# Optimization experiments

Hardware: AMD Instinct MI355X
Metric: run time of the kernel (lower is better)

The kernel has to match this reference:

```python
import jax, jax.numpy as jnp
import numpy as np

N = 100000      # nodes
E = 1600000     # edges (before self-loops)
NFEAT = 256
NHID = 64       # heads=1, concat -> output dim = NHID
NEG_SLOPE = 0.2 # PyG GATConv default negative_slope


def setup_inputs() -> dict:
    key = jax.random.key(0)
    k1, k2, k3, k4, k5 = jax.random.split(key, 5)
    x = jax.random.normal(k1, (N, NFEAT), dtype=jnp.float32)
    edge_index = jax.random.randint(k2, (2, E), 0, N, dtype=jnp.int64)
    s = 1.0 / np.sqrt(NFEAT)
    W = jax.random.uniform(k3, (NFEAT, NHID), jnp.float32, -s, s)      # lin weight
    a_src = jax.random.normal(k4, (NHID,), jnp.float32) * 0.1          # att_src
    a_dst = jax.random.normal(k5, (NHID,), jnp.float32) * 0.1          # att_dst
    bias = jnp.zeros((NHID,), jnp.float32)
    return {"x": x, "edge_index": edge_index, "W": W,
            "a_src": a_src, "a_dst": a_dst, "bias": bias}


def reference(x, edge_index, W, a_src, a_dst, bias):
    n = x.shape[0]
    xp = x @ W                                   # [N, NHID] transformed features
    # add self-loops (PyG default add_self_loops=True)
    loop = jnp.arange(n, dtype=edge_index.dtype)
    src = jnp.concatenate([edge_index[0], loop])  # message source j
    dst = jnp.concatenate([edge_index[1], loop])  # message target i
    # per-edge attention logits: LeakyReLU(a_src.x'_j + a_dst.x'_i)
    e = jax.nn.leaky_relu((xp @ a_src)[src] + (xp @ a_dst)[dst], NEG_SLOPE)  # [E+N]
    # segment softmax over incoming edges of each destination node
    m = jax.ops.segment_max(e, dst, num_segments=n)       # [N] (every node has a self-loop)
    ex = jnp.exp(e - m[dst])
    denom = jax.ops.segment_sum(ex, dst, num_segments=n)  # [N]
    alpha = ex / denom[dst]                                # [E+N]
    # attention-weighted scatter aggregation
    out = jax.ops.segment_sum(alpha[:, None] * xp[src], dst, num_segments=n)  # [N, NHID]
    return out + bias
```

## Files before the change

kernel.cpp:

```cpp
#include <hip/hip_runtime.h>
#include <hip/hip_bf16.h>

#define NFEAT 256
#define NHID  64
#define BSH   8
#define BUCKN 256
#define CAP   5120
#define CHUNK 4096

typedef unsigned int u32;
typedef unsigned short u16;
typedef long long ll;

typedef __attribute__((ext_vector_type(8))) short bf16x8;
typedef __attribute__((ext_vector_type(4))) float f32x4;

__device__ __forceinline__ float bfu2f(u16 u) {
    return __uint_as_float((u32)u << 16);
}
__device__ __forceinline__ u16 f2bfu(float f) {
    u32 u = __float_as_uint(f);
    u32 r = (u + 0x7fffu + ((u >> 16) & 1u)) >> 16;
    return (u16)r;
}
__device__ __forceinline__ float load_f(const void* p, int i, int f32) {
    return f32 ? ((const float*)p)[i] : bfu2f(((const u16*)p)[i]);
}

__device__ __forceinline__ void load_edge(const void* ei, int i64f, int E, int eid,
                                          int& src, int& dst) {
    if (eid < E) {
        if (i64f) {
            src = (int)((const ll*)ei)[eid];
            dst = (int)((const ll*)ei)[(size_t)E + eid];
        } else {
            src = ((const int*)ei)[eid];
            dst = ((const int*)ei)[(size_t)E + eid];
        }
    } else {
        src = dst = eid - E;
    }
}

__global__ __launch_bounds__(256) void prep_kernel(
    const void* __restrict__ W_, const void* __restrict__ ei,
    int* __restrict__ flags, u16* __restrict__ wt)
{
    __shared__ int f32sh;
    const int tid = threadIdx.x;
    if (tid == 0) f32sh = 0;
    __syncthreads();
    {
        float v = bfu2f(((const u16*)W_)[tid]);
        if (!(fabsf(v) <= 0.07f)) f32sh = 1;
    }
    if (tid < 64) {
        int v = ((const int*)ei)[2 * tid + 1];
        unsigned long long m = __ballot(v != 0);
        if (tid == 0) flags[1] = (m == 0ull) ? 1 : 0;
    }
    __syncthreads();
    const int f32 = f32sh;
    if (tid == 0) flags[0] = f32;
    for (int j = tid; j < NFEAT * NHID; j += 256) {
        int h = j >> 8, k = j & 255;
        wt[j] = f2bfu(load_f(W_, k * NHID + h, f32));
    }
}

__global__ __launch_bounds__(256) void gemm_kernel(
    const void* __restrict__ x_, const u16* __restrict__ wt,
    const void* __restrict__ a_src, const void* __restrict__ a_dst,
    const int* __restrict__ flags, u16* __restrict__ xpb,
    float* __restrict__ s, float* __restrict__ t_, int n)
{
    const int tid = threadIdx.x;
    const int lane = tid & 63;
    const int wv = tid >> 6;
    const int q = lane >> 4;
    const int l15 = lane & 15;
    const int f32 = flags[0];
    const int t = blockIdx.x;
    const int arow = min(t * 64 + wv * 16 + l15, n - 1);

    f32x4 acc[4] = {{0,0,0,0},{0,0,0,0},{0,0,0,0},{0,0,0,0}};
    const u16* wbase = wt + l15 * NFEAT + q * 8;

    if (f32) {
        const float* xb = (const float*)x_ + (size_t)arow * NFEAT + q * 8;
        #pragma unroll
        for (int ks = 0; ks < 8; ++ks) {
            float4 v0 = *(const float4*)(xb + ks * 32);
            float4 v1 = *(const float4*)(xb + ks * 32 + 4);
            bf16x8 a;
            a[0] = (short)f2bfu(v0.x); a[1] = (short)f2bfu(v0.y);
            a[2] = (short)f2bfu(v0.z); a[3] = (short)f2bfu(v0.w);
            a[4] = (short)f2bfu(v1.x); a[5] = (short)f2bfu(v1.y);
            a[6] = (short)f2bfu(v1.z); a[7] = (short)f2bfu(v1.w);
            #pragma unroll
            for (int tl = 0; tl < 4; ++tl) {
                bf16x8 b = *(const bf16x8*)(wbase + tl * 16 * NFEAT + ks * 32);
                acc[tl] = __builtin_amdgcn_mfma_f32_16x16x32_bf16(a, b, acc[tl], 0, 0, 0);
            }
        }
    } else {
        const u16* xb = (const u16*)x_ + (size_t)arow * NFEAT + q * 8;
        #pragma unroll
        for (int ks = 0; ks < 8; ++ks) {
            bf16x8 a = *(const bf16x8*)(xb + ks * 32);
            #pragma unroll
            for (int tl = 0; tl < 4; ++tl) {
                bf16x8 b = *(const bf16x8*)(wbase + tl * 16 * NFEAT + ks * 32);
                acc[tl] = __builtin_amdgcn_mfma_f32_16x16x32_bf16(a, b, acc[tl], 0, 0, 0);
            }
        }
    }

    float asl[4], adl[4];
    #pragma unroll
    for (int tl = 0; tl < 4; ++tl) {
        asl[tl] = load_f(a_src, tl * 16 + l15, f32);
        adl[tl] = load_f(a_dst, tl * 16 + l15, f32);
    }
    #pragma unroll
    for (int reg = 0; reg < 4; ++reg) {
        int node = t * 64 + wv * 16 + q * 4 + reg;
        bool ok = node < n;
        float pvs = 0.f, pvt = 0.f;
        #pragma unroll
        for (int tl = 0; tl < 4; ++tl) {
            float v = acc[tl][reg];
            if (ok) xpb[(size_t)node * NHID + tl * 16 + l15] = f2bfu(v);
            pvs = fmaf(v, asl[tl], pvs);
            pvt = fmaf(v, adl[tl], pvt);
        }
        #pragma unroll
        for (int o = 1; o < 16; o <<= 1) {
            pvs += __shfl_xor(pvs, o);
            pvt += __shfl_xor(pvt, o);
        }
        if (ok && l15 == 0) { s[node] = pvs; t_[node] = pvt; }
    }
}

__global__ __launch_bounds__(512) void bucket_kernel(
    const void* __restrict__ ei, const int* __restrict__ flags,
    int* __restrict__ gcursor, u32* __restrict__ rec, int E, int total)
{
    __shared__ int hist[512];
    __shared__ int offs[512];
    __shared__ int curs[512];
    __shared__ int gbase[512];
    __shared__ u32 stage[CHUNK];
    const int tid = threadIdx.x;
    const int base = blockIdx.x * CHUNK;
    const int cn = min(CHUNK, total - base);
    const int i64f = flags[1];

    hist[tid] = 0;
    __syncthreads();
    int es[8], ed[8];
    #pragma unroll
    for (int j = 0; j < 8; ++j) {
        int e = base + tid + 512 * j;
        if (e < total) {
            load_edge(ei, i64f, E, e, es[j], ed[j]);
            atomicAdd(&hist[ed[j] >> BSH], 1);
        } else ed[j] = -1;
    }
    __syncthreads();
    int v = hist[tid];
    offs[tid] = v;
    __syncthreads();
    for (int o = 1; o < 512; o <<= 1) {
        int tv = (tid >= o) ? offs[tid - o] : 0;
        __syncthreads();
        offs[tid] += tv;
        __syncthreads();
    }
    int excl = offs[tid] - v;
    __syncthreads();
    offs[tid] = excl;
    curs[tid] = excl;
    __syncthreads();
    #pragma unroll
    for (int j = 0; j < 8; ++j) {
        if (ed[j] >= 0) {
            int b = ed[j] >> BSH;
            int p = atomicAdd(&curs[b], 1);
            stage[p] = ((u32)(ed[j] & 255) << 24) | (u32)es[j];
        }
    }
    __syncthreads();
    {
        int b = tid;
        int nxt = (b < 511) ? offs[b + 1] : cn;
        int cb = nxt - offs[b];
        gbase[b] = b * CAP + (cb ? atomicAdd(&gcursor[b], cb) : 0);
    }
    __syncthreads();
    for (int i = tid; i < cn; i += 512) {
        u32 r = stage[i];
        int lo = 0, hi = 511;
        while (lo < hi) {
            int mid = (lo + hi + 1) >> 1;
            if (offs[mid] <= i) lo = mid; else hi = mid - 1;
        }
        rec[(size_t)gbase[lo] + (i - offs[lo])] = r;
    }
}

#define HN 128
__global__ __launch_bounds__(512) void fused_kernel(
    const u32* __restrict__ rec, const int* __restrict__ gcursor,
    const float* __restrict__ s, const float* __restrict__ t_,
    const u16* __restrict__ xpb, const void* __restrict__ bias,
    const int* __restrict__ flags, float* __restrict__ out, int n)
{
    __shared__ int rowp[HN + 1];
    __shared__ int curs[HN];
    __shared__ int ssrc[CAP * 3 / 4];
    const int b = blockIdx.x >> 1;
    const int half = blockIdx.x & 1;
    const int tid = threadIdx.x;
    const int dst0 = (b << BSH) + half * HN;
    const int cnt = min(gcursor[b], CAP);
    const u32* r = rec + (size_t)b * CAP;
    const int SCAP = CAP * 3 / 4;

    for (int i = tid; i <= HN; i += 512) rowp[i] = 0;
    __syncthreads();
    for (int i = tid; i < cnt; i += 512) {
        u32 v = r[i];
        int dl = (int)(v >> 24);
        if ((dl >> 7) == half) atomicAdd(&rowp[(dl & (HN - 1)) + 1], 1);
    }
    __syncthreads();
    for (int o = 1; o <= HN; o <<= 1) {
        int tv = 0;
        if (tid <= HN && tid >= o) tv = rowp[tid - o];
        __syncthreads();
        if (tid <= HN && tid >= o) rowp[tid] += tv;
        __syncthreads();
    }
    if (tid < HN) curs[tid] = rowp[tid];
    __syncthreads();
    for (int i = tid; i < cnt; i += 512) {
        u32 v = r[i];
        int dl = (int)(v >> 24);
        if ((dl >> 7) == half) {
            int p = atomicAdd(&curs[dl & (HN - 1)], 1);
            if (p < SCAP) ssrc[p] = (int)(v & 0x00FFFFFFu);
        }
    }
    __syncthreads();

    const int lane = tid & 63;
    const int wv = tid >> 6;
    const float bl = load_f(bias, lane, flags[0]);
    for (int nl = wv; nl < HN; nl += 8) {
        int node = dst0 + nl;
        if (node >= n) break;
        int beg = rowp[nl], end = min(rowp[nl + 1], SCAP);
        float tn = t_[node];
        float lsum = 0.f;
        float O0 = 0.f, O1 = 0.f, O2 = 0.f, O3 = 0.f;
        for (int j0 = beg; j0 < end; j0 += 64) {
            int c2 = min(64, end - j0);
            int sidx = 0; float p = 0.f;
            if (lane < c2) {
                sidx = ssrc[j0 + lane];
                float e = s[sidx] + tn;
                e = (e >= 0.f) ? e : 0.2f * e;
                p = __expf(e);
            }
            lsum += p;
            int jj = 0;
            for (; jj + 8 <= c2; jj += 8) {
                int sj[8]; float pj[8], rv[8];
                #pragma unroll
                for (int u = 0; u < 8; ++u) {
                    sj[u] = __shfl(sidx, jj + u);
                    pj[u] = __shfl(p, jj + u);
                }
                #pragma unroll
                for (int u = 0; u < 8; ++u)
                    rv[u] = bfu2f(xpb[(size_t)sj[u] * NHID + lane]);
                O0 = fmaf(pj[0], rv[0], O0); O1 = fmaf(pj[1], rv[1], O1);
                O2 = fmaf(pj[2], rv[2], O2); O3 = fmaf(pj[3], rv[3], O3);
                O0 = fmaf(pj[4], rv[4], O0); O1 = fmaf(pj[5], rv[5], O1);
                O2 = fmaf(pj[6], rv[6], O2); O3 = fmaf(pj[7], rv[7], O3);
            }
            for (; jj < c2; ++jj) {
                int s0 = __shfl(sidx, jj);
                float p0 = __shfl(p, jj);
                O0 = fmaf(p0, bfu2f(xpb[(size_t)s0 * NHID + lane]), O0);
            }
        }
        #pragma unroll
        for (int o = 32; o; o >>= 1) lsum += __shfl_xor(lsum, o);
        out[(size_t)node * NHID + lane] = ((O0 + O1) + (O2 + O3)) / lsum + bl;
    }
}

extern "C" void kernel_launch(void* const* d_in, const int* in_sizes, int n_in,
                              void* d_out, int out_size, void* d_ws, size_t ws_size,
                              hipStream_t stream) {
    const void* x     = d_in[0];
    const void* ei    = d_in[1];
    const void* W     = d_in[2];
    const void* a_src = d_in[3];
    const void* a_dst = d_in[4];
    const void* bias  = d_in[5];
    float* out = (float*)d_out;

    const int n     = in_sizes[0] / NFEAT;
    const int E     = in_sizes[1] / 2;
    const int total = E + n;
    const int NB    = (n + BUCKN - 1) >> BSH;
    const int NT    = (n + 63) / 64;

    char* ws = (char*)d_ws;
    size_t off = 0;
    auto carve = [&](size_t bytes) -> char* {
        char* p = ws + off;
        off = (off + bytes + 255) & ~(size_t)255;
        return p;
    };
    int*   flags   = (int*)  carve(64 * sizeof(int));
    u16*   wt      = (u16*)  carve((size_t)NFEAT * NHID * 2);
    u16*   xpb     = (u16*)  carve((size_t)n * NHID * 2);
    float* s       = (float*)carve((size_t)n * 4);
    float* t       = (float*)carve((size_t)n * 4);
    int*   gcursor = (int*)  carve(512 * 4);
    u32*   rec     = (u32*)  carve((size_t)NB * CAP * 4);

    hipMemsetAsync(gcursor, 0, 512 * 4, stream);

    prep_kernel<<<1, 256, 0, stream>>>(W, ei, flags, wt);
    gemm_kernel<<<NT, 256, 0, stream>>>(x, wt, a_src, a_dst, flags, xpb, s, t, n);
    bucket_kernel<<<(total + CHUNK - 1) / CHUNK, 512, 0, stream>>>(ei, flags, gcursor, rec, E, total);
    fused_kernel<<<NB * 2, 512, 0, stream>>>(rec, gcursor, s, t, xpb, bias, flags, out, n);
}
```

Measured before the change: 301.5 us.

## Replace bucketed edge staging with full CSR build via global count, scan, scatter

Replaces the two-level bucket sort (fixed-capacity buckets of 256 destinations, re-sorted in shared memory by each aggregation block) with a standard CSR construction. A global atomic degree count, a three-kernel prefix scan and a global atomic scatter produce per-node edge lists. The aggregation kernel then uses one wavefront per node in a grid-stride loop, reading sources straight from global memory. This removes the capacity truncation and the in-block sorting, but adds four extra launches and scattered global atomics on 100k counters, and edge order within a node becomes nondeterministic.

New measurement: 452.9 us. 1.5x slower.

```diff
diff --git a/kernel.cpp b/kernel.cpp
--- a/kernel.cpp
+++ b/kernel.cpp
@@ -3,10 +3,6 @@
 
 #define NFEAT 256
 #define NHID  64
-#define BSH   8
-#define BUCKN 256
-#define CAP   5120
-#define CHUNK 4096
 
 typedef unsigned int u32;
 typedef unsigned short u16;
@@ -143,133 +139,110 @@
     }
 }
 
-__global__ __launch_bounds__(512) void bucket_kernel(
+__global__ __launch_bounds__(256) void count_kernel(
     const void* __restrict__ ei, const int* __restrict__ flags,
-    int* __restrict__ gcursor, u32* __restrict__ rec, int E, int total)
-{
-    __shared__ int hist[512];
-    __shared__ int offs[512];
-    __shared__ int curs[512];
-    __shared__ int gbase[512];
-    __shared__ u32 stage[CHUNK];
-    const int tid = threadIdx.x;
-    const int base = blockIdx.x * CHUNK;
-    const int cn = min(CHUNK, total - base);
+    int* __restrict__ cnt, int E)
+{
     const int i64f = flags[1];
-
-    hist[tid] = 0;
-    __syncthreads();
-    int es[8], ed[8];
-    #pragma unroll
-    for (int j = 0; j < 8; ++j) {
-        int e = base + tid + 512 * j;
-        if (e < total) {
-            load_edge(ei, i64f, E, e, es[j], ed[j]);
-            atomicAdd(&hist[ed[j] >> BSH], 1);
-        } else ed[j] = -1;
-    }
-    __syncthreads();
-    int v = hist[tid];
-    offs[tid] = v;
+    const int stride = gridDim.x * 256;
+    for (int e = blockIdx.x * 256 + threadIdx.x; e < E; e += stride) {
+        int dst = i64f ? (int)((const ll*)ei)[(size_t)E + e]
+                       : ((const int*)ei)[(size_t)E + e];
+        atomicAdd(&cnt[dst], 1);
+    }
+}
+
+__global__ __launch_bounds__(256) void scan1_kernel(
+    const int* __restrict__ cnt, int* __restrict__ bsum, int n)
+{
+    __shared__ int sh[256];
+    const int t = threadIdx.x;
+    const int v = blockIdx.x * 256 + t;
+    sh[t] = (v < n) ? cnt[v] + 1 : 0;
+    __syncthreads();
+    for (int o = 128; o; o >>= 1) {
+        if (t < o) sh[t] += sh[t + o];
+        __syncthreads();
+    }
+    if (t == 0) bsum[blockIdx.x] = sh[0];
+}
+
+__global__ __launch_bounds__(512) void scan2_kernel(
+    const int* __restrict__ bsum, int* __restrict__ coff, int nc)
+{
+    __shared__ int sh[512];
+    const int t = threadIdx.x;
+    int mine = (t < nc) ? bsum[t] : 0;
+    sh[t] = mine;
     __syncthreads();
     for (int o = 1; o < 512; o <<= 1) {
-        int tv = (tid >= o) ? offs[tid - o] : 0;
-        __syncthreads();
-        offs[tid] += tv;
-        __syncthreads();
-    }
-    int excl = offs[tid] - v;
-    __syncthreads();
-    offs[tid] = excl;
-    curs[tid] = excl;
-    __syncthreads();
-    #pragma unroll
-    for (int j = 0; j < 8; ++j) {
-        if (ed[j] >= 0) {
-            int b = ed[j] >> BSH;
-            int p = atomicAdd(&curs[b], 1);
-            stage[p] = ((u32)(ed[j] & 255) << 24) | (u32)es[j];
-        }
-    }
-    __syncthreads();
-    {
-        int b = tid;
-        int nxt = (b < 511) ? offs[b + 1] : cn;
-        int cb = nxt - offs[b];
-        gbase[b] = b * CAP + (cb ? atomicAdd(&gcursor[b], cb) : 0);
-    }
-    __syncthreads();
-    for (int i = tid; i < cn; i += 512) {
-        u32 r = stage[i];
-        int lo = 0, hi = 511;
-        while (lo < hi) {
-            int mid = (lo + hi + 1) >> 1;
-            if (offs[mid] <= i) lo = mid; else hi = mid - 1;
-        }
-        rec[(size_t)gbase[lo] + (i - offs[lo])] = r;
-    }
-}
-
-#define HN 128
-__global__ __launch_bounds__(512) void fused_kernel(
-    const u32* __restrict__ rec, const int* __restrict__ gcursor,
+        int v = (t >= o) ? sh[t - o] : 0;
+        __syncthreads();
+        sh[t] += v;
+        __syncthreads();
+    }
+    if (t < nc) coff[t] = sh[t] - mine;
+}
+
+__global__ __launch_bounds__(256) void scan3_kernel(
+    const int* __restrict__ cnt, const int* __restrict__ coff,
+    int* __restrict__ base, int* __restrict__ cur, int n)
+{
+    __shared__ int sh[256];
+    const int t = threadIdx.x;
+    const int v = blockIdx.x * 256 + t;
+    int d = (v < n) ? cnt[v] + 1 : 0;
+    sh[t] = d;
+    __syncthreads();
+    for (int o = 1; o < 256; o <<= 1) {
+        int x = (t >= o) ? sh[t - o] : 0;
+        __syncthreads();
+        sh[t] += x;
+        __syncthreads();
+    }
+    if (v < n) {
+        int b = coff[blockIdx.x] + sh[t] - d;
+        base[v] = b;
+        cur[v] = b;
+    }
+}
+
+__global__ __launch_bounds__(256) void scatter_kernel(
+    const void* __restrict__ ei, const int* __restrict__ flags,
+    int* __restrict__ cur, u32* __restrict__ rec, int E, int total)
+{
+    const int i64f = flags[1];
+    const int stride = gridDim.x * 256;
+    for (int e = blockIdx.x * 256 + threadIdx.x; e < total; e += stride) {
+        int src, dst;
+        load_edge(ei, i64f, E, e, src, dst);
+        int p = atomicAdd(&cur[dst], 1);
+        rec[p] = (u32)src;
+    }
+}
+
+__global__ __launch_bounds__(256) void fused_kernel(
+    const u32* __restrict__ rec, const int* __restrict__ base,
+    const int* __restrict__ cur,
     const float* __restrict__ s, const float* __restrict__ t_,
     const u16* __restrict__ xpb, const void* __restrict__ bias,
     const int* __restrict__ flags, float* __restrict__ out, int n)
 {
-    __shared__ int rowp[HN + 1];
-    __shared__ int curs[HN];
-    __shared__ int ssrc[CAP * 3 / 4];
-    const int b = blockIdx.x >> 1;
-    const int half = blockIdx.x & 1;
-    const int tid = threadIdx.x;
-    const int dst0 = (b << BSH) + half * HN;
-    const int cnt = min(gcursor[b], CAP);
-    const u32* r = rec + (size_t)b * CAP;
-    const int SCAP = CAP * 3 / 4;
-
-    for (int i = tid; i <= HN; i += 512) rowp[i] = 0;
-    __syncthreads();
-    for (int i = tid; i < cnt; i += 512) {
-        u32 v = r[i];
-        int dl = (int)(v >> 24);
-        if ((dl >> 7) == half) atomicAdd(&rowp[(dl & (HN - 1)) + 1], 1);
-    }
-    __syncthreads();
-    for (int o = 1; o <= HN; o <<= 1) {
-        int tv = 0;
-        if (tid <= HN && tid >= o) tv = rowp[tid - o];
-        __syncthreads();
-        if (tid <= HN && tid >= o) rowp[tid] += tv;
-        __syncthreads();
-    }
-    if (tid < HN) curs[tid] = rowp[tid];
-    __syncthreads();
-    for (int i = tid; i < cnt; i += 512) {
-        u32 v = r[i];
-        int dl = (int)(v >> 24);
-        if ((dl >> 7) == half) {
-            int p = atomicAdd(&curs[dl & (HN - 1)], 1);
-            if (p < SCAP) ssrc[p] = (int)(v & 0x00FFFFFFu);
-        }
-    }
-    __syncthreads();
-
-    const int lane = tid & 63;
-    const int wv = tid >> 6;
+    const int lane = threadIdx.x & 63;
+    const int wid = blockIdx.x * (blockDim.x >> 6) + (threadIdx.x >> 6);
+    const int nw = gridDim.x * (blockDim.x >> 6);
     const float bl = load_f(bias, lane, flags[0]);
-    for (int nl = wv; nl < HN; nl += 8) {
-        int node = dst0 + nl;
-        if (node >= n) break;
-        int beg = rowp[nl], end = min(rowp[nl + 1], SCAP);
-        float tn = t_[node];
+
+    for (int node = wid; node < n; node += nw) {
+        const int beg = base[node], end = cur[node];
+        const float tn = t_[node];
         float lsum = 0.f;
         float O0 = 0.f, O1 = 0.f, O2 = 0.f, O3 = 0.f;
         for (int j0 = beg; j0 < end; j0 += 64) {
             int c2 = min(64, end - j0);
             int sidx = 0; float p = 0.f;
             if (lane < c2) {
-                sidx = ssrc[j0 + lane];
+                sidx = (int)rec[j0 + lane];
                 float e = s[sidx] + tn;
                 e = (e >= 0.f) ? e : 0.2f * e;
                 p = __expf(e);
@@ -317,8 +290,8 @@
     const int n     = in_sizes[0] / NFEAT;
     const int E     = in_sizes[1] / 2;
     const int total = E + n;
-    const int NB    = (n + BUCKN - 1) >> BSH;
     const int NT    = (n + 63) / 64;
+    const int NC    = (n + 255) / 256;
 
     char* ws = (char*)d_ws;
     size_t off = 0;
@@ -327,18 +300,26 @@
         off = (off + bytes + 255) & ~(size_t)255;
         return p;
     };
-    int*   flags   = (int*)  carve(64 * sizeof(int));
-    u16*   wt      = (u16*)  carve((size_t)NFEAT * NHID * 2);
-    u16*   xpb     = (u16*)  carve((size_t)n * NHID * 2);
-    float* s       = (float*)carve((size_t)n * 4);
-    float* t       = (float*)carve((size_t)n * 4);
-    int*   gcursor = (int*)  carve(512 * 4);
-    u32*   rec     = (u32*)  carve((size_t)NB * CAP * 4);
-
-    hipMemsetAsync(gcursor, 0, 512 * 4, stream);
+    int*   flags = (int*)  carve(64 * sizeof(int));
+    u16*   wt    = (u16*)  carve((size_t)NFEAT * NHID * 2);
+    u16*   xpb   = (u16*)  carve((size_t)n * NHID * 2);
+    float* s     = (float*)carve((size_t)n * 4);
+    float* t     = (float*)carve((size_t)n * 4);
+    int*   cnt   = (int*)  carve((size_t)n * 4);
+    int*   base  = (int*)  carve((size_t)n * 4);
+    int*   cur   = (int*)  carve((size_t)n * 4);
+    int*   bsum  = (int*)  carve(512 * 4);
+    int*   coff  = (int*)  carve(512 * 4);
+    u32*   rec   = (u32*)  carve((size_t)total * 4);
+
+    hipMemsetAsync(cnt, 0, (size_t)n * 4, stream);
 
     prep_kernel<<<1, 256, 0, stream>>>(W, ei, flags, wt);
     gemm_kernel<<<NT, 256, 0, stream>>>(x, wt, a_src, a_dst, flags, xpb, s, t, n);
-    bucket_kernel<<<(total + CHUNK - 1) / CHUNK, 512, 0, stream>>>(ei, flags, gcursor, rec, E, total);
-    fused_kernel<<<NB * 2, 512, 0, stream>>>(rec, gcursor, s, t, xpb, bias, flags, out, n);
-}
+    count_kernel<<<2048, 256, 0, stream>>>(ei, flags, cnt, E);
+    scan1_kernel<<<NC, 256, 0, stream>>>(cnt, bsum, n);
+    scan2_kernel<<<1, 512, 0, stream>>>(bsum, coff, NC);
+    scan3_kernel<<<NC, 256, 0, stream>>>(cnt, coff, base, cur, n);
+    scatter_kernel<<<2048, 256, 0, stream>>>(ei, flags, cur, rec, E, total);
+    fused_kernel<<<2048, 256, 0, stream>>>(rec, base, cur, s, t, xpb, bias, flags, out, n);
+}
```
